# Optimization experiments

Measured on AMD Instinct MI355X. Metric: run time of the kernel, lower is better.

## Reference

```python
import jax, jax.numpy as jnp
import numpy as np

SIGMAS = jnp.array([0.0001, 0.001, 0.01, 0.1, 1, 5, 10, 15, 20, 25, 30, 100], dtype=jnp.float32)


def setup_inputs() -> dict:
    key = jax.random.key(0)
    k1, k2 = jax.random.split(key)
    N, D = 4096, 256
    feature = jax.random.normal(k1, (N, D), dtype=jnp.float32)
    domain = jax.random.randint(k2, (N,), 0, 8, dtype=jnp.int64)
    return {"feature": feature, "domain": domain}


def reference(feature, domain):
    # Pairwise squared L2 distances via the Gram trick (avoids NxNxD intermediate).
    sq = jnp.sum(feature * feature, axis=1)            # [N]
    gram = feature @ feature.T                          # [N, N]
    d2 = jnp.maximum(sq[:, None] + sq[None, :] - 2.0 * gram, 0.0)  # [N, N]

    # Multi-sigma Gaussian kernel sum: sum_s exp(-d2/2 * s). Loop over the
    # small fixed set of 12 sigmas to avoid a 12xNxN intermediate.
    k = jnp.zeros_like(d2)
    for s in [0.0001, 0.001, 0.01, 0.1, 1.0, 5.0, 10.0, 15.0, 20.0, 25.0, 30.0, 100.0]:
        k = k + jnp.exp(-d2 * (0.5 * s))

    same = (domain[:, None] == domain[None, :]).astype(jnp.float32)  # [N, N]
    neg = 1.0 - same
    Ex = jnp.sum(same * k) / jnp.sum(same)
    Ey = jnp.sum(neg * k) / jnp.sum(neg)
    return Ex - Ey
```

## Files before the change

kernel.cpp:

```cpp
#include <hip/hip_runtime.h>


typedef __attribute__((ext_vector_type(8))) short short8;
typedef __attribute__((ext_vector_type(4))) float floatx4;

#define AS1 __attribute__((address_space(1)))
#define AS3 __attribute__((address_space(3)))

__device__ inline unsigned f2bf2(float lo, float hi) {
  union { float f; unsigned u; } a, b; a.f = lo; b.f = hi;
  unsigned ra = (a.u + 0x7fffu + ((a.u >> 16) & 1u)) >> 16;
  unsigned rb = (b.u + 0x7fffu + ((b.u >> 16) & 1u)) >> 16;
  return ra | (rb << 16);
}

__device__ inline float fast_exp2(float x) {
#if __has_builtin(__builtin_amdgcn_exp2f)
  return __builtin_amdgcn_exp2f(x);
#else
  return exp2f(x);
#endif
}

__global__ __launch_bounds__(256) void prep_kernel(
    const float* __restrict__ feat, uint4* __restrict__ fbt,
    float* __restrict__ sqpart, int N, int D) {
  const int tid = threadIdx.x;
  const int rt = blockIdx.x >> 2;
  const int kq = blockIdx.x & 3;
  const int r = tid & 63;
  const int nkc = D >> 3;
  __shared__ float sqp[256];
  float ss = 0.f;
  #pragma unroll
  for (int it = 0; it < 2; ++it) {
    const int kc = kq * 8 + it * 4 + (tid >> 6);
    const float4* src = (const float4*)(feat + (size_t)(rt * 64 + r) * D + kc * 8);
    float4 v0 = src[0], v1 = src[1];
    ss += v0.x*v0.x + v0.y*v0.y + v0.z*v0.z + v0.w*v0.w
        + v1.x*v1.x + v1.y*v1.y + v1.z*v1.z + v1.w*v1.w;
    uint4 o;
    o.x = f2bf2(v0.x, v0.y); o.y = f2bf2(v0.z, v0.w);
    o.z = f2bf2(v1.x, v1.y); o.w = f2bf2(v1.z, v1.w);
    fbt[(size_t)rt * nkc * 64 + kc * 64 + r] = o;
  }
  sqp[tid] = ss;
  __syncthreads();
  if (tid < 64)
    sqpart[(size_t)kq * N + rt * 64 + tid] =
        sqp[tid] + sqp[tid + 64] + sqp[tid + 128] + sqp[tid + 192];
}

__global__ __launch_bounds__(256) void mmd_main(
    const uint4* __restrict__ fbt, const float* __restrict__ sqpart,
    const int* __restrict__ dom, float2* __restrict__ partial, int N) {
  int b = blockIdx.x;
  int i = (int)((sqrtf(8.f * (float)b + 1.f) - 1.f) * 0.5f);
  while ((i + 1) * (i + 2) / 2 <= b) ++i;
  while (i * (i + 1) / 2 > b) --i;
  const int ti = b - i * (i + 1) / 2;
  const int tj = i;
  const int rowI = ti * 64, rowJ = tj * 64;

  __shared__ __align__(16) uint4 Bs[2048];
  __shared__ float sqI[64], sqJ[64];
  __shared__ int dmI[64], dmJ[64];
  __shared__ float red[8];

  const int tid = threadIdx.x;
  const int lane = tid & 63, w = tid >> 6;
  const int quad = lane >> 4, m16 = lane & 15;

  const uint4* At = fbt + (size_t)ti * 2048;
  const uint4* Bt = fbt + (size_t)tj * 2048;

  #pragma unroll
  for (int p = 0; p < 8; ++p) {
    const int base = w * 64 + p * 256;
#if __has_builtin(__builtin_amdgcn_global_load_lds)
    __builtin_amdgcn_global_load_lds(
        (const AS1 uint4*)(Bt + base + lane),
        (AS3 uint4*)(Bs + base), 16, 0, 0);
#else
    Bs[base + lane] = Bt[base + lane];
#endif
  }

  short8 afrag[8];
  #pragma unroll
  for (int s = 0; s < 8; ++s) {
    uint4 t = At[(s * 4 + quad) * 64 + w * 16 + m16];
    afrag[s] = *(short8*)&t;
  }

  if (tid < 64) {
    sqI[tid] = sqpart[rowI + tid] + sqpart[N + rowI + tid]
             + sqpart[2 * N + rowI + tid] + sqpart[3 * N + rowI + tid];
    dmI[tid] = dom[rowI + tid];
  } else if (tid < 128) {
    int t = tid - 64;
    sqJ[t] = sqpart[rowJ + t] + sqpart[N + rowJ + t]
           + sqpart[2 * N + rowJ + t] + sqpart[3 * N + rowJ + t];
    dmJ[t] = dom[rowJ + t];
  }
  __syncthreads();

  floatx4 acc[4];
  #pragma unroll
  for (int t = 0; t < 4; ++t) acc[t] = (floatx4){0.f, 0.f, 0.f, 0.f};

  const unsigned short* BsS = (const unsigned short*)Bs;
  #pragma unroll
  for (int s = 0; s < 8; ++s) {
    #pragma unroll
    for (int t = 0; t < 4; ++t) {
      short8 bf = *(const short8*)(BsS + ((size_t)((s * 4 + quad) * 64 + t * 16 + m16)) * 8);
      acc[t] = __builtin_amdgcn_mfma_f32_16x16x32_bf16(afrag[s], bf, acc[t], 0, 0, 0);
    }
  }

  const float C0 = -7.2134752e-05f, C1 = -7.2134752e-04f, C2 = -7.2134752e-03f,
              C3 = -7.2134752e-02f, C4 = -0.72134752f, C5 = -3.6067376f,
              C100 = -72.13475204f;

  float s_all = 0.f, s_same = 0.f;
  #pragma unroll
  for (int t = 0; t < 4; ++t) {
    const int c = t * 16 + m16;
    const float sqc = sqJ[c];
    const int dc = dmJ[c];
    const int gj = rowJ + c;
    #pragma unroll
    for (int reg = 0; reg < 4; ++reg) {
      const int r = w * 16 + quad * 4 + reg;
      const int gi = rowI + r;
      float d2 = sqI[r] + sqc - 2.f * acc[t][reg];
      d2 = fmaxf(d2, 0.f);
      if (gi == gj) d2 = 0.f;
      float e0 = fast_exp2(d2 * C0), e1 = fast_exp2(d2 * C1);
      float e2 = fast_exp2(d2 * C2), e3 = fast_exp2(d2 * C3);
      float e4 = fast_exp2(d2 * C4), e5 = fast_exp2(d2 * C5);
      float e11 = fast_exp2(d2 * C100);
      float t10 = e5 * e5, t15 = t10 * e5, t20 = t10 * t10;
      float t25 = t15 * t10, t30 = t15 * t15;
      float kk = ((e0 + e1) + (e2 + e3)) + ((e4 + e5) + (t10 + t15))
               + ((t20 + t25) + (t30 + e11));
      s_all += kk;
      if (dmI[r] == dc) s_same += kk;
    }
  }
  #pragma unroll
  for (int off = 32; off > 0; off >>= 1) {
    s_all  += __shfl_down(s_all, off);
    s_same += __shfl_down(s_same, off);
  }
  if (lane == 0) { red[w] = s_all; red[4 + w] = s_same; }
  __syncthreads();
  if (tid == 0) {
    const float wt = (ti == tj) ? 1.f : 2.f;
    float a = (red[0] + red[1] + red[2] + red[3]) * wt;
    float s = (red[4] + red[5] + red[6] + red[7]) * wt;
    partial[b] = make_float2(s, a);
  }
}

__global__ __launch_bounds__(256) void finalize_kernel(
    const float2* __restrict__ partial, int nblk,
    const int* __restrict__ dom, float* __restrict__ out, int N) {
  __shared__ int histL[16];
  __shared__ double redS[8];
  const int tid = threadIdx.x;
  if (tid < 16) histL[tid] = 0;
  __syncthreads();
  for (int i = tid; i < N; i += 256) atomicAdd(&histL[dom[i] & 15], 1);
  double as = 0.0, aa = 0.0;
  for (int i = tid; i < nblk; i += 256) {
    float2 p = partial[i];
    as += (double)p.x; aa += (double)p.y;
  }
  #pragma unroll
  for (int off = 32; off > 0; off >>= 1) {
    as += __shfl_down(as, off);
    aa += __shfl_down(aa, off);
  }
  const int w = tid >> 6;
  if ((tid & 63) == 0) { redS[w] = as; redS[4 + w] = aa; }
  __syncthreads();
  if (tid == 0) {
    double S = redS[0] + redS[1] + redS[2] + redS[3];
    double A = redS[4] + redS[5] + redS[6] + redS[7];
    double csame = 0.0;
    for (int i = 0; i < 16; ++i) { double h = (double)histL[i]; csame += h * h; }
    double call = (double)N * (double)N;
    out[0] = (float)(S / csame - (A - S) / (call - csame));
  }
}

extern "C" void kernel_launch(void* const* d_in, const int* in_sizes, int n_in,
                              void* d_out, int out_size, void* d_ws, size_t ws_size,
                              hipStream_t stream) {
  const float* feat = (const float*)d_in[0];
  const int* dom = (const int*)d_in[1];
  float* out = (float*)d_out;
  const int N = in_sizes[1];
  const int D = in_sizes[0] / N;
  const int T = N / 64;
  const int nblk = T * (T + 1) / 2;

  char* ws = (char*)d_ws;
  float2* partial = (float2*)ws;
  float* sqpart = (float*)(ws + 16640);
  uint4* fbt = (uint4*)(ws + 82176);

  prep_kernel<<<dim3(T * 4), dim3(256), 0, stream>>>(feat, fbt, sqpart, N, D);
  mmd_main<<<dim3(nblk), dim3(256), 0, stream>>>(fbt, sqpart, dom, partial, N);
  finalize_kernel<<<1, 256, 0, stream>>>(partial, nblk, dom, out, N);
}
```

Measured before the change: 81.45 us.

## Enlarge main-kernel tile to 128x128 with 512 threads per block

```diff
diff --git a/kernel.cpp b/kernel.cpp
--- a/kernel.cpp
+++ b/kernel.cpp
@@ -51,7 +51,7 @@
         sqp[tid] + sqp[tid + 64] + sqp[tid + 128] + sqp[tid + 192];
 }
 
-__global__ __launch_bounds__(256) void mmd_main(
+__global__ __launch_bounds__(512, 4) void mmd_main(
     const uint4* __restrict__ fbt, const float* __restrict__ sqpart,
     const int* __restrict__ dom, float2* __restrict__ partial, int N) {
   int b = blockIdx.x;
@@ -60,23 +60,23 @@
   while (i * (i + 1) / 2 > b) --i;
   const int ti = b - i * (i + 1) / 2;
   const int tj = i;
-  const int rowI = ti * 64, rowJ = tj * 64;
-
-  __shared__ __align__(16) uint4 Bs[2048];
-  __shared__ float sqI[64], sqJ[64];
-  __shared__ int dmI[64], dmJ[64];
-  __shared__ float red[8];
+  const int rowI = ti * 128, rowJ = tj * 128;
+
+  __shared__ __align__(16) uint4 Bs[4096];
+  __shared__ float sqI[128], sqJ[128];
+  __shared__ int dmI[128], dmJ[128];
+  __shared__ float red[16];
 
   const int tid = threadIdx.x;
   const int lane = tid & 63, w = tid >> 6;
   const int quad = lane >> 4, m16 = lane & 15;
 
-  const uint4* At = fbt + (size_t)ti * 2048;
-  const uint4* Bt = fbt + (size_t)tj * 2048;
+  const uint4* At = fbt + (size_t)ti * 4096;
+  const uint4* Bt = fbt + (size_t)tj * 4096;
 
   #pragma unroll
   for (int p = 0; p < 8; ++p) {
-    const int base = w * 64 + p * 256;
+    const int base = p * 512 + w * 64;
 #if __has_builtin(__builtin_amdgcn_global_load_lds)
     __builtin_amdgcn_global_load_lds(
         (const AS1 uint4*)(Bt + base + lane),
@@ -87,35 +87,40 @@
   }
 
   short8 afrag[8];
-  #pragma unroll
-  for (int s = 0; s < 8; ++s) {
-    uint4 t = At[(s * 4 + quad) * 64 + w * 16 + m16];
-    afrag[s] = *(short8*)&t;
-  }
-
-  if (tid < 64) {
+  {
+    const uint4* Aw = At + (size_t)(w >> 2) * 2048 + (w & 3) * 16 + m16;
+    #pragma unroll
+    for (int s = 0; s < 8; ++s) {
+      uint4 t = Aw[(s * 4 + quad) * 64];
+      afrag[s] = *(short8*)&t;
+    }
+  }
+
+  if (tid < 128) {
     sqI[tid] = sqpart[rowI + tid] + sqpart[N + rowI + tid]
              + sqpart[2 * N + rowI + tid] + sqpart[3 * N + rowI + tid];
     dmI[tid] = dom[rowI + tid];
-  } else if (tid < 128) {
-    int t = tid - 64;
+  } else if (tid < 256) {
+    int t = tid - 128;
     sqJ[t] = sqpart[rowJ + t] + sqpart[N + rowJ + t]
            + sqpart[2 * N + rowJ + t] + sqpart[3 * N + rowJ + t];
     dmJ[t] = dom[rowJ + t];
   }
   __syncthreads();
 
-  floatx4 acc[4];
-  #pragma unroll
-  for (int t = 0; t < 4; ++t) acc[t] = (floatx4){0.f, 0.f, 0.f, 0.f};
-
-  const unsigned short* BsS = (const unsigned short*)Bs;
+  floatx4 acc[8];
+  #pragma unroll
+  for (int t = 0; t < 8; ++t) acc[t] = (floatx4){0.f, 0.f, 0.f, 0.f};
+
   #pragma unroll
   for (int s = 0; s < 8; ++s) {
     #pragma unroll
-    for (int t = 0; t < 4; ++t) {
-      short8 bf = *(const short8*)(BsS + ((size_t)((s * 4 + quad) * 64 + t * 16 + m16)) * 8);
-      acc[t] = __builtin_amdgcn_mfma_f32_16x16x32_bf16(afrag[s], bf, acc[t], 0, 0, 0);
+    for (int t = 0; t < 8; ++t) {
+      const uint4* bp = Bs + (size_t)(t >> 2) * 2048
+                      + (s * 4 + quad) * 64 + (t & 3) * 16 + m16;
+      uint4 bt = *bp;
+      acc[t] = __builtin_amdgcn_mfma_f32_16x16x32_bf16(
+                   afrag[s], *(short8*)&bt, acc[t], 0, 0, 0);
     }
   }
 
@@ -124,17 +129,21 @@
               C100 = -72.13475204f;
 
   float s_all = 0.f, s_same = 0.f;
-  #pragma unroll
-  for (int t = 0; t < 4; ++t) {
+  const int r0 = w * 16 + quad * 4;
+  float sqr[4]; int dmr[4];
+  #pragma unroll
+  for (int reg = 0; reg < 4; ++reg) { sqr[reg] = sqI[r0 + reg]; dmr[reg] = dmI[r0 + reg]; }
+
+  #pragma unroll
+  for (int t = 0; t < 8; ++t) {
     const int c = t * 16 + m16;
     const float sqc = sqJ[c];
     const int dc = dmJ[c];
     const int gj = rowJ + c;
     #pragma unroll
     for (int reg = 0; reg < 4; ++reg) {
-      const int r = w * 16 + quad * 4 + reg;
-      const int gi = rowI + r;
-      float d2 = sqI[r] + sqc - 2.f * acc[t][reg];
+      const int gi = rowI + r0 + reg;
+      float d2 = sqr[reg] + sqc - 2.f * acc[t][reg];
       d2 = fmaxf(d2, 0.f);
       if (gi == gj) d2 = 0.f;
       float e0 = fast_exp2(d2 * C0), e1 = fast_exp2(d2 * C1);
@@ -146,7 +155,7 @@
       float kk = ((e0 + e1) + (e2 + e3)) + ((e4 + e5) + (t10 + t15))
                + ((t20 + t25) + (t30 + e11));
       s_all += kk;
-      if (dmI[r] == dc) s_same += kk;
+      if (dmr[reg] == dc) s_same += kk;
     }
   }
   #pragma unroll
@@ -154,13 +163,14 @@
     s_all  += __shfl_down(s_all, off);
     s_same += __shfl_down(s_same, off);
   }
-  if (lane == 0) { red[w] = s_all; red[4 + w] = s_same; }
+  if (lane == 0) { red[w] = s_all; red[8 + w] = s_same; }
   __syncthreads();
   if (tid == 0) {
     const float wt = (ti == tj) ? 1.f : 2.f;
-    float a = (red[0] + red[1] + red[2] + red[3]) * wt;
-    float s = (red[4] + red[5] + red[6] + red[7]) * wt;
-    partial[b] = make_float2(s, a);
+    float a = 0.f, s = 0.f;
+    #pragma unroll
+    for (int k = 0; k < 8; ++k) { a += red[k]; s += red[8 + k]; }
+    partial[b] = make_float2(s * wt, a * wt);
   }
 }
 
@@ -204,7 +214,7 @@
   float* out = (float*)d_out;
   const int N = in_sizes[1];
   const int D = in_sizes[0] / N;
-  const int T = N / 64;
+  const int T = N / 128;
   const int nblk = T * (T + 1) / 2;
 
   char* ws = (char*)d_ws;
@@ -212,7 +222,7 @@
   float* sqpart = (float*)(ws + 16640);
   uint4* fbt = (uint4*)(ws + 82176);
 
-  prep_kernel<<<dim3(T * 4), dim3(256), 0, stream>>>(feat, fbt, sqpart, N, D);
-  mmd_main<<<dim3(nblk), dim3(256), 0, stream>>>(fbt, sqpart, dom, partial, N);
+  prep_kernel<<<dim3((N / 64) * 4), dim3(256), 0, stream>>>(feat, fbt, sqpart, N, D);
+  mmd_main<<<dim3(nblk), dim3(512), 0, stream>>>(fbt, sqpart, dom, partial, N);
   finalize_kernel<<<1, 256, 0, stream>>>(partial, nblk, dom, out, N);
 }
```

Result: slower. 83.53 us (+2.6%).
